# Performance work log

Measured on AMD Instinct MI355X. Metric: run time of the kernel, lower is better.

## Reference

```python
import jax, jax.numpy as jnp
import numpy as np

N = 100000   # nodes
E = 1600000  # edges
D = 64       # in_channel == out_channel
NEG_SLOPE = 0.01  # nn.LeakyReLU default


def gcn_conv(x, W, b, src, dst, n):
    # PyG GCNConv: add self-loops, sym-normalize by in-degree (at col/dst),
    # norm(e) = deg[src]^-1/2 * deg[dst]^-1/2, aggregate at dst, then + bias.
    deg = jnp.zeros((n,), x.dtype).at[dst].add(1.0) + 1.0  # in-degree incl. self-loop
    dinv = jax.lax.rsqrt(deg)
    h = x @ W                                   # [N, Dout]
    coef = (dinv[src] * dinv[dst])[:, None]     # [E, 1]
    agg = jax.ops.segment_sum(h[src] * coef, dst, num_segments=n)  # scatter-add
    # self-loop contribution: deg[i]^-1 * h[i]
    return agg + (dinv * dinv)[:, None] * h + b


def setup_inputs() -> dict:
    key = jax.random.key(0)
    ks = jax.random.split(key, 10)
    x = jax.random.normal(ks[0], (N, D), dtype=jnp.float32)
    edge_index = jax.random.randint(ks[1], (2, E), 0, N)
    s = 1.0 / np.sqrt(D)  # glorot-ish scale
    inp = {"x": x, "edge_index": edge_index}
    for i in range(4):
        inp[f"W{i+1}"] = jax.random.normal(ks[2 + i], (D, D), dtype=jnp.float32) * s
        inp[f"b{i+1}"] = jnp.zeros((D,), dtype=jnp.float32)
    return inp


def reference(x, edge_index, W1, b1, W2, b2, W3, b3, W4, b4):
    # eval mode: F.dropout(training=False) is identity, so omitted.
    src, dst = edge_index[0], edge_index[1]
    h = x
    for W, b in ((W1, b1), (W2, b2), (W3, b3), (W4, b4)):
        h = gcn_conv(h, W, b, src, dst, N)
        h = jnp.where(h >= 0, h, NEG_SLOPE * h)  # LeakyReLU
    return h
```

## Files before the change

kernel.cpp:

```cpp
#include <hip/hip_runtime.h>
#include <hip/hip_fp16.h>

#define N_NODES 100000
#define N_EDGES 1600000
#define DIM 64
#define NEG_SLOPE 0.01f

#define BNODES 128
#define NBUCK 782
#define BCAP 4096
#define BLOCKS1 256
#define THREADS1 1024
#define EPB (N_EDGES / BLOCKS1)

typedef _Float16 half8 __attribute__((ext_vector_type(8)));
typedef float float4v __attribute__((ext_vector_type(4)));

__global__ void prep_weights(const float* __restrict__ W0, const float* __restrict__ W1,
                             const float* __restrict__ W2, const float* __restrict__ W3,
                             __half* __restrict__ WT16) {
    const float* Ws[4] = {W0, W1, W2, W3};
    const float* W = Ws[blockIdx.x];
    __half* dst = WT16 + (size_t)blockIdx.x * DIM * DIM;
    for (int e = threadIdx.x; e < DIM * DIM; e += 256) {
        int k = e >> 6, f = e & 63;
        dst[f * DIM + k] = __float2half(W[e]);
    }
}

__global__ __launch_bounds__(THREADS1) void bucket_scatter(const int* __restrict__ src,
                                                           const int* __restrict__ dst,
                                                           int* __restrict__ gcur,
                                                           int* __restrict__ bdata) {
    __shared__ int cnt[NBUCK];
    __shared__ int cur[NBUCK];
    __shared__ int lexcl[NBUCK];
    __shared__ int base[NBUCK];
    __shared__ int scan[THREADS1];
    __shared__ int sorted_e[EPB];
    __shared__ unsigned short sorted_b[EPB];

    const int tid = threadIdx.x;
    for (int i = tid; i < NBUCK; i += THREADS1) { cnt[i] = 0; cur[i] = 0; }
    __syncthreads();

    const int e0 = blockIdx.x * EPB;
    const int e1 = e0 + EPB;

    for (int e = e0 + tid; e < e1; e += THREADS1)
        atomicAdd(&cnt[dst[e] >> 7], 1);
    __syncthreads();

    int v = (tid < NBUCK) ? cnt[tid] : 0;
    scan[tid] = v;
    __syncthreads();
    for (int s = 1; s < THREADS1; s <<= 1) {
        int a = (tid >= s) ? scan[tid - s] : 0;
        __syncthreads();
        scan[tid] += a;
        __syncthreads();
    }
    if (tid < NBUCK) lexcl[tid] = scan[tid] - v;

    if (tid < NBUCK) {
        int c = cnt[tid];
        base[tid] = c ? atomicAdd(&gcur[tid * 16], c) : 0;
    }
    __syncthreads();

    for (int e = e0 + tid; e < e1; e += THREADS1) {
        int d = dst[e];
        int b = d >> 7;
        int p = lexcl[b] + atomicAdd(&cur[b], 1);
        sorted_e[p] = src[e] | ((d & 127) << 17);
        sorted_b[p] = (unsigned short)b;
    }
    __syncthreads();

    for (int i = tid; i < EPB; i += THREADS1) {
        int b = sorted_b[i];
        bdata[(size_t)b * BCAP + base[b] + (i - lexcl[b])] = sorted_e[i];
    }
}

__global__ void bucket_scan(const int* __restrict__ gcur, int* __restrict__ bbase) {
    __shared__ int sm[1024];
    const int tid = threadIdx.x;
    int v = (tid < NBUCK) ? gcur[tid * 16] : 0;
    sm[tid] = v;
    __syncthreads();
    for (int s = 1; s < 1024; s <<= 1) {
        int a = ((int)tid >= s) ? sm[tid - s] : 0;
        __syncthreads();
        sm[tid] += a;
        __syncthreads();
    }
    if (tid < NBUCK) bbase[tid] = sm[tid] - v;
}

__global__ __launch_bounds__(256) void bucket_build(const int* __restrict__ bdata,
                                                    const int* __restrict__ gcur,
                                                    const int* __restrict__ bbase,
                                                    int* __restrict__ offsets,
                                                    float* __restrict__ dinv,
                                                    int* __restrict__ csr) {
    __shared__ int cnt[BNODES];
    __shared__ int excl[BNODES];
    const int tid = threadIdx.x;
    const int b = blockIdx.x;
    const int sz = gcur[b * 16];
    const int* bd = bdata + (size_t)b * BCAP;
    const int cbase = bbase[b];

    for (int i = tid; i < BNODES; i += 256) cnt[i] = 0;
    __syncthreads();
    for (int i = tid; i < sz; i += 256)
        atomicAdd(&cnt[bd[i] >> 17], 1);
    __syncthreads();
    if (tid == 0) {
        int run = 0;
        for (int j = 0; j < BNODES; ++j) { excl[j] = run; run += cnt[j]; }
    }
    __syncthreads();

    const int nb = b * BNODES;
    for (int i = tid; i < BNODES; i += 256) {
        int n = nb + i;
        if (n < N_NODES) {
            offsets[n] = cbase + excl[i];
            dinv[n] = rsqrtf((float)(cnt[i] + 1));
        }
    }
    if (b == NBUCK - 1 && tid == 0) offsets[N_NODES] = N_EDGES;

    for (int i = tid; i < BNODES; i += 256) cnt[i] = 0;
    __syncthreads();
    for (int i = tid; i < sz; i += 256) {
        int v = bd[i];
        int l = v >> 17;
        int pos = cbase + excl[l] + atomicAdd(&cnt[l], 1);
        csr[pos] = (v & 0x1FFFF) << 6;
    }
}

__device__ __forceinline__ void stage8(__half* dst, const float* __restrict__ X, size_t off) {
    float4 f0 = *(const float4*)(X + off);
    float4 f1 = *(const float4*)(X + off + 4);
    __half2 h0 = __floats2half2_rn(f0.x, f0.y);
    __half2 h1 = __floats2half2_rn(f0.z, f0.w);
    __half2 h2 = __floats2half2_rn(f1.x, f1.y);
    __half2 h3 = __floats2half2_rn(f1.z, f1.w);
    uint4 u;
    u.x = *(unsigned int*)&h0; u.y = *(unsigned int*)&h1;
    u.z = *(unsigned int*)&h2; u.w = *(unsigned int*)&h3;
    *(uint4*)dst = u;
}
__device__ __forceinline__ void stage8(__half* dst, const __half* __restrict__ X, size_t off) {
    *(uint4*)dst = *(const uint4*)(X + off);
}

#define XPAD 72
template <typename TIN>
__global__ __launch_bounds__(256) void mm_kernel(const TIN* __restrict__ X,
                                                 const __half* __restrict__ WT,
                                                 const float* __restrict__ dinv,
                                                 __half* __restrict__ G16) {
    __shared__ __align__(16) __half xs[64][XPAD];
    __shared__ __align__(16) __half ws[64][XPAD];
    const int t = threadIdx.x;
    const int rbase = blockIdx.x * 64;

    for (int c = t; c < 512; c += 256) {
        int row = c >> 3, koff = (c & 7) * 8;
        int grow = rbase + row;
        if (grow < N_NODES) {
            stage8(&xs[row][koff], X, (size_t)grow * DIM + koff);
        } else {
            *(uint4*)&xs[row][koff] = make_uint4(0, 0, 0, 0);
        }
        stage8(&ws[row][koff], WT, (size_t)row * DIM + koff);
    }
    __syncthreads();

    const int wave = t >> 6;
    const int lane = t & 63;
    const int q = lane >> 4;
    const int c16 = lane & 15;
    const int n0 = wave * 16;

    half8 b0 = *(const half8*)&xs[n0 + c16][q * 8];
    half8 b1 = *(const half8*)&xs[n0 + c16][32 + q * 8];

    const int gnode = rbase + n0 + c16;
    float di = (gnode < N_NODES) ? dinv[gnode] : 0.f;

#pragma unroll
    for (int ft = 0; ft < 4; ++ft) {
        const int f0 = ft * 16;
        half8 a0 = *(const half8*)&ws[f0 + c16][q * 8];
        half8 a1 = *(const half8*)&ws[f0 + c16][32 + q * 8];
        float4v acc = {0.f, 0.f, 0.f, 0.f};
        acc = __builtin_amdgcn_mfma_f32_16x16x32_f16(a0, b0, acc, 0, 0, 0);
        acc = __builtin_amdgcn_mfma_f32_16x16x32_f16(a1, b1, acc, 0, 0, 0);
        if (gnode < N_NODES) {
            __half2 p0 = __floats2half2_rn(di * acc[0], di * acc[1]);
            __half2 p1 = __floats2half2_rn(di * acc[2], di * acc[3]);
            uint2 u;
            u.x = *(unsigned int*)&p0;
            u.y = *(unsigned int*)&p1;
            *(uint2*)(G16 + (size_t)gnode * DIM + f0 + q * 4) = u;
        }
    }
}

#define AGG_BLOCKS 2048
#define AGG_WAVES (AGG_BLOCKS * 4)
template <bool FINAL>
__global__ __launch_bounds__(256) void agg_kernel(const __half* __restrict__ G16,
                                                  const int* __restrict__ csr,
                                                  const int* __restrict__ offsets,
                                                  const float* __restrict__ dinv,
                                                  const float* __restrict__ bias,
                                                  void* __restrict__ outp) {
    const int gw = (blockIdx.x * 256 + threadIdx.x) >> 6;
    const int lane = threadIdx.x & 63;
    const int slot = lane >> 3;
    const int sub  = lane & 7;
    const int fc   = sub * 8;

    for (int wid = gw; wid < N_NODES; wid += AGG_WAVES) {
        const int beg = offsets[wid], end = offsets[wid + 1];

        __half2 h0 = __float2half2_rn(0.f), h1 = h0, h2 = h0, h3 = h0;

#define PKACC(vraw)                                     \
        {                                               \
            const __half2* hp = (const __half2*)&(vraw);\
            h0 = __hadd2(h0, hp[0]);                    \
            h1 = __hadd2(h1, hp[1]);                    \
            h2 = __hadd2(h2, hp[2]);                    \
            h3 = __hadd2(h3, hp[3]);                    \
        }

        int e = beg + slot;
        for (; e + 8 < end; e += 16) {
            int p0 = csr[e];
            int p1 = csr[e + 8];
            float4 v0 = *(const float4*)(G16 + (size_t)p0 + fc);
            float4 v1 = *(const float4*)(G16 + (size_t)p1 + fc);
            PKACC(v0)
            PKACC(v1)
        }
        if (e < end) {
            int p0 = csr[e];
            float4 v0 = *(const float4*)(G16 + (size_t)p0 + fc);
            PKACC(v0)
        }
#undef PKACC

        float acc[8];
        {
            float2 f;
            f = __half22float2(h0); acc[0] = f.x; acc[1] = f.y;
            f = __half22float2(h1); acc[2] = f.x; acc[3] = f.y;
            f = __half22float2(h2); acc[4] = f.x; acc[5] = f.y;
            f = __half22float2(h3); acc[6] = f.x; acc[7] = f.y;
        }
#pragma unroll
        for (int k = 0; k < 8; ++k) {
            acc[k] += __shfl_xor(acc[k], 8, 64);
            acc[k] += __shfl_xor(acc[k], 16, 64);
            acc[k] += __shfl_xor(acc[k], 32, 64);
        }

        if (slot == 0) {
            float4 vs = *(const float4*)(G16 + (size_t)wid * DIM + fc);
            {
                const __half2* hp = (const __half2*)&vs;
                float2 f0 = __half22float2(hp[0]);
                float2 f1 = __half22float2(hp[1]);
                float2 f2 = __half22float2(hp[2]);
                float2 f3 = __half22float2(hp[3]);
                acc[0] += f0.x; acc[1] += f0.y;
                acc[2] += f1.x; acc[3] += f1.y;
                acc[4] += f2.x; acc[5] += f2.y;
                acc[6] += f3.x; acc[7] += f3.y;
            }

            float di = dinv[wid];
            float4 b0 = *(const float4*)(bias + fc);
            float4 b1 = *(const float4*)(bias + fc + 4);
            float r[8];
            r[0] = di * acc[0] + b0.x;
            r[1] = di * acc[1] + b0.y;
            r[2] = di * acc[2] + b0.z;
            r[3] = di * acc[3] + b0.w;
            r[4] = di * acc[4] + b1.x;
            r[5] = di * acc[5] + b1.y;
            r[6] = di * acc[6] + b1.z;
            r[7] = di * acc[7] + b1.w;
#pragma unroll
            for (int k = 0; k < 8; ++k)
                r[k] = (r[k] >= 0.f) ? r[k] : NEG_SLOPE * r[k];

            if (FINAL) {
                float* out = (float*)outp;
                *(float4*)(out + (size_t)wid * DIM + fc)     = make_float4(r[0], r[1], r[2], r[3]);
                *(float4*)(out + (size_t)wid * DIM + fc + 4) = make_float4(r[4], r[5], r[6], r[7]);
            } else {
                __half* act = (__half*)outp;
                __half2 q0 = __floats2half2_rn(r[0], r[1]);
                __half2 q1 = __floats2half2_rn(r[2], r[3]);
                __half2 q2 = __floats2half2_rn(r[4], r[5]);
                __half2 q3 = __floats2half2_rn(r[6], r[7]);
                uint4 u;
                u.x = *(unsigned int*)&q0;
                u.y = *(unsigned int*)&q1;
                u.z = *(unsigned int*)&q2;
                u.w = *(unsigned int*)&q3;
                *(uint4*)(act + (size_t)wid * DIM + fc) = u;
            }
        }
    }
}

extern "C" void kernel_launch(void* const* d_in, const int* in_sizes, int n_in,
                              void* d_out, int out_size, void* d_ws, size_t ws_size,
                              hipStream_t stream) {
    const float* x = (const float*)d_in[0];
    const int* ei = (const int*)d_in[1];
    const int* src = ei;
    const int* dst = ei + N_EDGES;
    const float* W[4] = {(const float*)d_in[2], (const float*)d_in[4],
                         (const float*)d_in[6], (const float*)d_in[8]};
    const float* b[4] = {(const float*)d_in[3], (const float*)d_in[5],
                         (const float*)d_in[7], (const float*)d_in[9]};
    float* out = (float*)d_out;

    char* ws = (char*)d_ws;
    size_t off = 0;
    auto alloc = [&](size_t bytes) -> void* {
        void* p = ws + off;
        off = (off + bytes + 255) & ~(size_t)255;
        return p;
    };
    __half* G16   = (__half*)alloc((size_t)N_NODES * DIM * sizeof(__half));
    __half* ACT16 = (__half*)alloc((size_t)N_NODES * DIM * sizeof(__half));
    __half* WT16  = (__half*)alloc((size_t)4 * DIM * DIM * sizeof(__half));
    int*   csr    = (int*)alloc((size_t)N_EDGES * sizeof(int));
    int*   bdata  = (int*)alloc((size_t)NBUCK * BCAP * sizeof(int));
    int*   gcur   = (int*)alloc((size_t)NBUCK * 16 * sizeof(int));
    int*   bbase  = (int*)alloc((size_t)(NBUCK + 1) * sizeof(int));
    int*   offsets= (int*)alloc((size_t)(N_NODES + 1) * sizeof(int));
    float* dinv   = (float*)alloc((size_t)N_NODES * sizeof(float));

    hipMemsetAsync(gcur, 0, (size_t)NBUCK * 16 * sizeof(int), stream);
    prep_weights<<<4, 256, 0, stream>>>(W[0], W[1], W[2], W[3], WT16);

    bucket_scatter<<<BLOCKS1, THREADS1, 0, stream>>>(src, dst, gcur, bdata);
    bucket_scan<<<1, 1024, 0, stream>>>(gcur, bbase);
    bucket_build<<<NBUCK, 256, 0, stream>>>(bdata, gcur, bbase, offsets, dinv, csr);

    const int MM_GRID = (N_NODES + 63) / 64;

    mm_kernel<float><<<MM_GRID, 256, 0, stream>>>(x, WT16, dinv, G16);
    agg_kernel<false><<<AGG_BLOCKS, 256, 0, stream>>>(G16, csr, offsets, dinv, b[0], ACT16);
    mm_kernel<__half><<<MM_GRID, 256, 0, stream>>>(ACT16, WT16 + DIM * DIM, dinv, G16);
    agg_kernel<false><<<AGG_BLOCKS, 256, 0, stream>>>(G16, csr, offsets, dinv, b[1], ACT16);
    mm_kernel<__half><<<MM_GRID, 256, 0, stream>>>(ACT16, WT16 + 2 * DIM * DIM, dinv, G16);
    agg_kernel<false><<<AGG_BLOCKS, 256, 0, stream>>>(G16, csr, offsets, dinv, b[2], ACT16);
    mm_kernel<__half><<<MM_GRID, 256, 0, stream>>>(ACT16, WT16 + 3 * DIM * DIM, dinv, G16);
    agg_kernel<true><<<AGG_BLOCKS, 256, 0, stream>>>(G16, csr, offsets, dinv, b[3], out);
}
```

Measured before the change: 337.4 us.

## Fuse aggregation with next layer's matmul via per-wave LDS activation tiles

Merges each layer's neighbor aggregation with the following layer's 64x64 transform. Each wave aggregates 16 nodes into an LDS tile, then applies MFMA against the next weight matrix and writes pre-scaled features directly. This removes three standalone matmul kernels and the fp16 activation round trip through global memory, using ping-pong feature buffers. In exchange the grid changes from a persistent grid-stride loop to a fixed 16 nodes per wave, which can worsen load balance across uneven degrees and adds LDS use per block.

```diff
diff --git a/kernel.cpp b/kernel.cpp
--- a/kernel.cpp
+++ b/kernel.cpp
@@ -160,8 +160,7 @@
 }
 
 #define XPAD 72
-template <typename TIN>
-__global__ __launch_bounds__(256) void mm_kernel(const TIN* __restrict__ X,
+__global__ __launch_bounds__(256) void mm_kernel(const float* __restrict__ X,
                                                  const __half* __restrict__ WT,
                                                  const float* __restrict__ dinv,
                                                  __half* __restrict__ G16) {
@@ -213,22 +212,34 @@
     }
 }
 
-#define AGG_BLOCKS 2048
-#define AGG_WAVES (AGG_BLOCKS * 4)
 template <bool FINAL>
-__global__ __launch_bounds__(256) void agg_kernel(const __half* __restrict__ G16,
-                                                  const int* __restrict__ csr,
-                                                  const int* __restrict__ offsets,
-                                                  const float* __restrict__ dinv,
-                                                  const float* __restrict__ bias,
-                                                  void* __restrict__ outp) {
-    const int gw = (blockIdx.x * 256 + threadIdx.x) >> 6;
-    const int lane = threadIdx.x & 63;
+__global__ __launch_bounds__(256) void aggmm_kernel(const __half* __restrict__ Gin,
+                                                    const int* __restrict__ csr,
+                                                    const int* __restrict__ offsets,
+                                                    const float* __restrict__ dinv,
+                                                    const float* __restrict__ bias,
+                                                    const __half* __restrict__ WT,
+                                                    void* __restrict__ outp) {
+    __shared__ __align__(16) __half ws[64][XPAD];
+    __shared__ __align__(16) __half act[4][16][XPAD];
+    const int t = threadIdx.x;
+    const int wave = t >> 6;
+    const int lane = t & 63;
+
+    if (!FINAL) {
+        for (int c = t; c < 512; c += 256)
+            stage8(&ws[c >> 3][(c & 7) * 8], WT, (size_t)(c >> 3) * DIM + (c & 7) * 8);
+        __syncthreads();
+    }
+
     const int slot = lane >> 3;
     const int sub  = lane & 7;
     const int fc   = sub * 8;
-
-    for (int wid = gw; wid < N_NODES; wid += AGG_WAVES) {
+    const int tileBase = blockIdx.x * 64 + wave * 16;
+
+    for (int i = 0; i < 16; ++i) {
+        const int wid = tileBase + i;
+        if (wid >= N_NODES) break;
         const int beg = offsets[wid], end = offsets[wid + 1];
 
         __half2 h0 = __float2half2_rn(0.f), h1 = h0, h2 = h0, h3 = h0;
@@ -241,19 +252,18 @@
             h2 = __hadd2(h2, hp[2]);                    \
             h3 = __hadd2(h3, hp[3]);                    \
         }
-
         int e = beg + slot;
         for (; e + 8 < end; e += 16) {
             int p0 = csr[e];
             int p1 = csr[e + 8];
-            float4 v0 = *(const float4*)(G16 + (size_t)p0 + fc);
-            float4 v1 = *(const float4*)(G16 + (size_t)p1 + fc);
+            float4 v0 = *(const float4*)(Gin + (size_t)p0 + fc);
+            float4 v1 = *(const float4*)(Gin + (size_t)p1 + fc);
             PKACC(v0)
             PKACC(v1)
         }
         if (e < end) {
             int p0 = csr[e];
-            float4 v0 = *(const float4*)(G16 + (size_t)p0 + fc);
+            float4 v0 = *(const float4*)(Gin + (size_t)p0 + fc);
             PKACC(v0)
         }
 #undef PKACC
@@ -274,7 +284,7 @@
         }
 
         if (slot == 0) {
-            float4 vs = *(const float4*)(G16 + (size_t)wid * DIM + fc);
+            float4 vs = *(const float4*)(Gin + (size_t)wid * DIM + fc);
             {
                 const __half2* hp = (const __half2*)&vs;
                 float2 f0 = __half22float2(hp[0]);
@@ -286,7 +296,6 @@
                 acc[4] += f2.x; acc[5] += f2.y;
                 acc[6] += f3.x; acc[7] += f3.y;
             }
-
             float di = dinv[wid];
             float4 b0 = *(const float4*)(bias + fc);
             float4 b1 = *(const float4*)(bias + fc + 4);
@@ -308,7 +317,6 @@
                 *(float4*)(out + (size_t)wid * DIM + fc)     = make_float4(r[0], r[1], r[2], r[3]);
                 *(float4*)(out + (size_t)wid * DIM + fc + 4) = make_float4(r[4], r[5], r[6], r[7]);
             } else {
-                __half* act = (__half*)outp;
                 __half2 q0 = __floats2half2_rn(r[0], r[1]);
                 __half2 q1 = __floats2half2_rn(r[2], r[3]);
                 __half2 q2 = __floats2half2_rn(r[4], r[5]);
@@ -318,8 +326,37 @@
                 u.y = *(unsigned int*)&q1;
                 u.z = *(unsigned int*)&q2;
                 u.w = *(unsigned int*)&q3;
-                *(uint4*)(act + (size_t)wid * DIM + fc) = u;
+                *(uint4*)&act[wave][i][fc] = u;
             }
+        }
+    }
+
+    if (FINAL) return;
+
+    const int q = lane >> 4;
+    const int c16 = lane & 15;
+    half8 b0 = *(const half8*)&act[wave][c16][q * 8];
+    half8 b1 = *(const half8*)&act[wave][c16][32 + q * 8];
+
+    const int gnode = tileBase + c16;
+    float di = (gnode < N_NODES) ? dinv[gnode] : 0.f;
+    __half* Gout = (__half*)outp;
+
+#pragma unroll
+    for (int ft = 0; ft < 4; ++ft) {
+        const int f0 = ft * 16;
+        half8 a0 = *(const half8*)&ws[f0 + c16][q * 8];
+        half8 a1 = *(const half8*)&ws[f0 + c16][32 + q * 8];
+        float4v acc = {0.f, 0.f, 0.f, 0.f};
+        acc = __builtin_amdgcn_mfma_f32_16x16x32_f16(a0, b0, acc, 0, 0, 0);
+        acc = __builtin_amdgcn_mfma_f32_16x16x32_f16(a1, b1, acc, 0, 0, 0);
+        if (gnode < N_NODES) {
+            __half2 p0 = __floats2half2_rn(di * acc[0], di * acc[1]);
+            __half2 p1 = __floats2half2_rn(di * acc[2], di * acc[3]);
+            uint2 u;
+            u.x = *(unsigned int*)&p0;
+            u.y = *(unsigned int*)&p1;
+            *(uint2*)(Gout + (size_t)gnode * DIM + f0 + q * 4) = u;
         }
     }
 }
@@ -344,8 +381,8 @@
         off = (off + bytes + 255) & ~(size_t)255;
         return p;
     };
-    __half* G16   = (__half*)alloc((size_t)N_NODES * DIM * sizeof(__half));
-    __half* ACT16 = (__half*)alloc((size_t)N_NODES * DIM * sizeof(__half));
+    __half* GA    = (__half*)alloc((size_t)N_NODES * DIM * sizeof(__half));
+    __half* GB    = (__half*)alloc((size_t)N_NODES * DIM * sizeof(__half));
     __half* WT16  = (__half*)alloc((size_t)4 * DIM * DIM * sizeof(__half));
     int*   csr    = (int*)alloc((size_t)N_EDGES * sizeof(int));
     int*   bdata  = (int*)alloc((size_t)NBUCK * BCAP * sizeof(int));
@@ -363,12 +400,13 @@
 
     const int MM_GRID = (N_NODES + 63) / 64;
 
-    mm_kernel<float><<<MM_GRID, 256, 0, stream>>>(x, WT16, dinv, G16);
-    agg_kernel<false><<<AGG_BLOCKS, 256, 0, stream>>>(G16, csr, offsets, dinv, b[0], ACT16);
-    mm_kernel<__half><<<MM_GRID, 256, 0, stream>>>(ACT16, WT16 + DIM * DIM, dinv, G16);
-    agg_kernel<false><<<AGG_BLOCKS, 256, 0, stream>>>(G16, csr, offsets, dinv, b[1], ACT16);
-    mm_kernel<__half><<<MM_GRID, 256, 0, stream>>>(ACT16, WT16 + 2 * DIM * DIM, dinv, G16);
-    agg_kernel<false><<<AGG_BLOCKS, 256, 0, stream>>>(G16, csr, offsets, dinv, b[2], ACT16);
-    mm_kernel<__half><<<MM_GRID, 256, 0, stream>>>(ACT16, WT16 + 3 * DIM * DIM, dinv, G16);
-    agg_kernel<true><<<AGG_BLOCKS, 256, 0, stream>>>(G16, csr, offsets, dinv, b[3], out);
-}
+    mm_kernel<<<MM_GRID, 256, 0, stream>>>(x, WT16, dinv, GA);
+    aggmm_kernel<false><<<MM_GRID, 256, 0, stream>>>(GA, csr, offsets, dinv, b[0],
+                                                     WT16 + DIM * DIM, GB);
+    aggmm_kernel<false><<<MM_GRID, 256, 0, stream>>>(GB, csr, offsets, dinv, b[1],
+                                                     WT16 + 2 * DIM * DIM, GA);
+    aggmm_kernel<false><<<MM_GRID, 256, 0, stream>>>(GA, csr, offsets, dinv, b[2],
+                                                     WT16 + 3 * DIM * DIM, GB);
+    aggmm_kernel<true><<<MM_GRID, 256, 0, stream>>>(GB, csr, offsets, dinv, b[3],
+                                                    nullptr, out);
+}
```

After: 342.8 us. About the same (+1.6%).

## Fold bucket scan into build kernel and aggregate two nodes per wave

Applied to the files above, without the earlier changes.

Removes the separate single-block bucket_scan launch: each bucket_build block now sums the sizes of all preceding buckets itself with a shared-memory reduction to get its base offset. The aggregation kernel is changed so each 64-lane wave handles two destination nodes (one per 32-lane half), with 4 edge slots per node instead of 8, dropping one shuffle stage. This aims to cut a launch and improve lane utilisation for low-degree nodes (average degree about 16), at the cost of redundant prefix reads in the build kernel.

```diff
diff --git a/kernel.cpp b/kernel.cpp
--- a/kernel.cpp
+++ b/kernel.cpp
@@ -83,34 +83,29 @@
     }
 }
 
-__global__ void bucket_scan(const int* __restrict__ gcur, int* __restrict__ bbase) {
-    __shared__ int sm[1024];
-    const int tid = threadIdx.x;
-    int v = (tid < NBUCK) ? gcur[tid * 16] : 0;
-    sm[tid] = v;
-    __syncthreads();
-    for (int s = 1; s < 1024; s <<= 1) {
-        int a = ((int)tid >= s) ? sm[tid - s] : 0;
-        __syncthreads();
-        sm[tid] += a;
-        __syncthreads();
-    }
-    if (tid < NBUCK) bbase[tid] = sm[tid] - v;
-}
-
 __global__ __launch_bounds__(256) void bucket_build(const int* __restrict__ bdata,
                                                     const int* __restrict__ gcur,
-                                                    const int* __restrict__ bbase,
                                                     int* __restrict__ offsets,
                                                     float* __restrict__ dinv,
                                                     int* __restrict__ csr) {
     __shared__ int cnt[BNODES];
     __shared__ int excl[BNODES];
+    __shared__ int part[256];
     const int tid = threadIdx.x;
     const int b = blockIdx.x;
     const int sz = gcur[b * 16];
     const int* bd = bdata + (size_t)b * BCAP;
-    const int cbase = bbase[b];
+
+    int s = 0;
+    for (int i = tid; i < b; i += 256) s += gcur[i * 16];
+    part[tid] = s;
+    __syncthreads();
+    for (int st = 128; st > 0; st >>= 1) {
+        if (tid < st) part[tid] += part[tid + st];
+        __syncthreads();
+    }
+    const int cbase = part[0];
+    __syncthreads();
 
     for (int i = tid; i < BNODES; i += 256) cnt[i] = 0;
     __syncthreads();
@@ -215,6 +210,7 @@
 
 #define AGG_BLOCKS 2048
 #define AGG_WAVES (AGG_BLOCKS * 4)
+#define NPAIRS (N_NODES / 2)
 template <bool FINAL>
 __global__ __launch_bounds__(256) void agg_kernel(const __half* __restrict__ G16,
                                                   const int* __restrict__ csr,
@@ -224,11 +220,13 @@
                                                   void* __restrict__ outp) {
     const int gw = (blockIdx.x * 256 + threadIdx.x) >> 6;
     const int lane = threadIdx.x & 63;
-    const int slot = lane >> 3;
+    const int grp  = lane >> 5;
+    const int slot = (lane >> 3) & 3;
     const int sub  = lane & 7;
     const int fc   = sub * 8;
 
-    for (int wid = gw; wid < N_NODES; wid += AGG_WAVES) {
+    for (int p = gw; p < NPAIRS; p += AGG_WAVES) {
+        const int wid = p * 2 + grp;
         const int beg = offsets[wid], end = offsets[wid + 1];
 
         __half2 h0 = __float2half2_rn(0.f), h1 = h0, h2 = h0, h3 = h0;
@@ -243,9 +241,9 @@
         }
 
         int e = beg + slot;
-        for (; e + 8 < end; e += 16) {
+        for (; e + 4 < end; e += 8) {
             int p0 = csr[e];
-            int p1 = csr[e + 8];
+            int p1 = csr[e + 4];
             float4 v0 = *(const float4*)(G16 + (size_t)p0 + fc);
             float4 v1 = *(const float4*)(G16 + (size_t)p1 + fc);
             PKACC(v0)
@@ -270,7 +268,6 @@
         for (int k = 0; k < 8; ++k) {
             acc[k] += __shfl_xor(acc[k], 8, 64);
             acc[k] += __shfl_xor(acc[k], 16, 64);
-            acc[k] += __shfl_xor(acc[k], 32, 64);
         }
 
         if (slot == 0) {
@@ -350,7 +347,6 @@
     int*   csr    = (int*)alloc((size_t)N_EDGES * sizeof(int));
     int*   bdata  = (int*)alloc((size_t)NBUCK * BCAP * sizeof(int));
     int*   gcur   = (int*)alloc((size_t)NBUCK * 16 * sizeof(int));
-    int*   bbase  = (int*)alloc((size_t)(NBUCK + 1) * sizeof(int));
     int*   offsets= (int*)alloc((size_t)(N_NODES + 1) * sizeof(int));
     float* dinv   = (float*)alloc((size_t)N_NODES * sizeof(float));
 
@@ -358,8 +354,7 @@
     prep_weights<<<4, 256, 0, stream>>>(W[0], W[1], W[2], W[3], WT16);
 
     bucket_scatter<<<BLOCKS1, THREADS1, 0, stream>>>(src, dst, gcur, bdata);
-    bucket_scan<<<1, 1024, 0, stream>>>(gcur, bbase);
-    bucket_build<<<NBUCK, 256, 0, stream>>>(bdata, gcur, bbase, offsets, dinv, csr);
+    bucket_build<<<NBUCK, 256, 0, stream>>>(bdata, gcur, offsets, dinv, csr);
 
     const int MM_GRID = (N_NODES + 63) / 64;
 
```

Result: faster. 308.0 us (-8.7%).
